# Performance work log

Hardware: AMD Instinct MI355X
Metric: run time of the kernel (lower is better)

## Reference

```python
import jax, jax.numpy as jnp
import numpy as np

DIRECTIONS = [(0, 0), (1, 0), (-1, 0), (0, 1), (0, -1)]  # (dx, dy)
BN_EPS = 1e-5


def shift2d(x, directions=DIRECTIONS):
    # x: (B, C, H, W). Split channels into G groups, roll each spatially,
    # zero out the wrapped-around border (zero_pad mode), then concat.
    C = x.shape[1]
    G = len(directions)
    base = C // G
    sizes = [base] * (G - 1) + [C - base * (G - 1)]
    starts = np.concatenate([[0], np.cumsum(sizes)])
    out = []
    for i, (dx, dy) in enumerate(directions):
        chunk = x[:, starts[i]:starts[i + 1]]
        if dx == 0 and dy == 0:
            out.append(chunk)
            continue
        y = jnp.roll(chunk, shift=(dy, dx), axis=(-2, -1))
        if dy > 0:
            y = y.at[..., :dy, :].set(0.0)
        elif dy < 0:
            y = y.at[..., dy:, :].set(0.0)
        if dx > 0:
            y = y.at[..., :, :dx].set(0.0)
        elif dx < 0:
            y = y.at[..., :, dx:].set(0.0)
        out.append(y)
    return jnp.concatenate(out, axis=1)


def setup_inputs() -> dict:
    key = jax.random.key(0)
    k1, k2, k3, k4 = jax.random.split(key, 4)
    B, Cin, Cout, H, W = 32, 256, 256, 56, 56
    x = jax.random.normal(k1, (B, Cin, H, W), dtype=jnp.float32)
    pw_w = jax.random.normal(k2, (Cout, Cin), dtype=jnp.float32) * (1.0 / np.sqrt(Cin))
    gamma = jnp.ones((Cout,), dtype=jnp.float32)
    beta = jnp.zeros((Cout,), dtype=jnp.float32)
    running_mean = jax.random.normal(k3, (Cout,), dtype=jnp.float32) * 0.1
    running_var = jax.random.uniform(k4, (Cout,), dtype=jnp.float32, minval=0.5, maxval=1.5)
    return {"x": x, "pw_w": pw_w, "gamma": gamma, "beta": beta,
            "running_mean": running_mean, "running_var": running_var}


def reference(x, pw_w, gamma, beta, running_mean, running_var):
    # Shift (parameter-free spatial mixing)
    y = shift2d(x)
    # stride=1 -> down is Identity
    # 1x1 conv (no bias): pointwise channel mixing
    y = jnp.einsum('bchw,oc->bohw', y, pw_w)
    # BatchNorm2d (inference form with running stats) + ReLU
    inv = gamma * jax.lax.rsqrt(running_var + BN_EPS)
    y = y * inv[None, :, None, None] + (beta - running_mean * inv)[None, :, None, None]
    return jax.nn.relu(y)
```

## Files before the change

kernel.cpp:

```cpp
#include <hip/hip_runtime.h>

#define H_ 56
#define W_ 56
#define HW_ 3136
#define CIN_ 256
#define COUT_ 256

typedef __attribute__((ext_vector_type(8))) short short8;
typedef __attribute__((ext_vector_type(4))) float f32x4;

__device__ unsigned short g_wbf[COUT_ * CIN_];

__device__ __forceinline__ int swz32(int n) { return ((n ^ (n >> 3)) & 3) << 3; }

__device__ __forceinline__ unsigned short f2bf(float f) {
  union { float f; unsigned int i; } v; v.f = f;
  unsigned int b = v.i + (0x7fffu + ((v.i >> 16) & 1u));
  return (unsigned short)(b >> 16);
}

__device__ __forceinline__ void gload_lds16(const unsigned short* g, unsigned short* l) {
  __builtin_amdgcn_global_load_lds(
      (const __attribute__((address_space(1))) unsigned int*)g,
      (__attribute__((address_space(3))) unsigned int*)l, 16, 0, 0);
}

__device__ __forceinline__ void shift_decode(int c, int& dx, int& dy) {
  if (c < 102)      { dy = 0; dx = (c < 51) ? 0 : 1; }
  else if (c < 153) { dx = -1; dy = 0; }
  else if (c < 204) { dx = 0;  dy = 1; }
  else              { dx = 0;  dy = -1; }
}

__global__ __launch_bounds__(256)
void prep_weights(const float* __restrict__ wgt) {
  int idx  = blockIdx.x * 256 + threadIdx.x;
  int tile = idx >> 12;
  int bm = tile >> 3, kt = tile & 7;
  int e   = idx & 4095;
  int m   = e >> 5, col = e & 31;
  int o   = bm * 128 + m;
  int k   = kt * 32 + (col ^ swz32(m));
  g_wbf[idx] = f2bf(wgt[o * CIN_ + k]);
}

__device__ __forceinline__ void load_x(const float* __restrict__ x, size_t xb,
                                       int hh, int w0, int c,
                                       float4& p0, float4& p1, float& pe) {
  int dx, dy; shift_decode(c, dx, dy);
  int h2 = hh - dy;
  p0 = make_float4(0.f, 0.f, 0.f, 0.f);
  p1 = make_float4(0.f, 0.f, 0.f, 0.f);
  pe = 0.f;
  if ((unsigned)h2 < (unsigned)H_) {
    const float* row = x + xb + (size_t)c * HW_ + h2 * W_;
    p0 = *(const float4*)(row + w0);
    p1 = *(const float4*)(row + w0 + 4);
    if (dx == 1)       { if (w0 > 0)      pe = row[w0 - 1]; }
    else if (dx == -1) { if (w0 + 8 < W_) pe = row[w0 + 8]; }
  }
}

__device__ __forceinline__ void write_b(unsigned short* __restrict__ B,
                                        int nloc0, int krow, int c,
                                        const float4& p0, const float4& p1, float pe) {
  int dx, dy; shift_decode(c, dx, dy);
  float s[8] = {p0.x, p0.y, p0.z, p0.w, p1.x, p1.y, p1.z, p1.w};
  float vals[8];
  if (dx == 0) {
    #pragma unroll
    for (int i = 0; i < 8; ++i) vals[i] = s[i];
  } else if (dx == 1) {
    #pragma unroll
    for (int i = 7; i >= 1; --i) vals[i] = s[i - 1];
    vals[0] = pe;
  } else {
    #pragma unroll
    for (int i = 0; i < 7; ++i) vals[i] = s[i + 1];
    vals[7] = pe;
  }
  #pragma unroll
  for (int i = 0; i < 8; ++i) {
    int nl = nloc0 + i;
    B[nl * 32 + (krow ^ swz32(nl))] = f2bf(vals[i]);
  }
}

__global__ __launch_bounds__(256, 6)
void shiftconv_gemm(const float* __restrict__ x,
                    const float* __restrict__ gamma,
                    const float* __restrict__ beta,
                    const float* __restrict__ rmean,
                    const float* __restrict__ rvar,
                    float* __restrict__ out)
{
  __shared__ unsigned short Alds[2][128 * 32];
  __shared__ unsigned short Blds[2][64 * 32];
  __shared__ float bnp[256];

  const int t = threadIdx.x;
  const int orig = blockIdx.x;
  const int wgid = (orig & 7) * 392 + (orig >> 3);
  const int bm   = wgid & 1;
  const int bn   = wgid >> 1;

  const int lane = t & 63;
  const int wv   = t >> 6;
  const int wm   = wv >> 1;
  const int wn   = wv & 1;
  const int quad = lane >> 4;
  const int l15  = lane & 15;

  if (t < 128) {
    int o = bm * 128 + t;
    float inv = gamma[o] * rsqrtf(rvar[o] + 1e-5f);
    bnp[2 * t]     = inv;
    bnp[2 * t + 1] = beta[o] - rmean[o] * inv;
  }

  const int chunk  = t & 7;
  const int krow   = t >> 3;
  const int nloc0  = chunk * 8;
  const int nglob0 = bn * 64 + nloc0;
  const int bidx   = nglob0 / HW_;
  const int rem    = nglob0 - bidx * HW_;
  const int hh     = rem / W_;
  const int w0     = rem - hh * W_;
  const size_t xb  = (size_t)bidx * CIN_ * HW_;

  const unsigned short* wsrc = g_wbf + bm * (8 * 4096) + t * 8;

  f32x4 acc[4][2];
  #pragma unroll
  for (int i = 0; i < 4; ++i)
    #pragma unroll
    for (int j = 0; j < 2; ++j)
      acc[i][j] = (f32x4){0.f, 0.f, 0.f, 0.f};

  float4 p0, p1;
  float  pe;

  {
    const unsigned short* g = wsrc;
    gload_lds16(g,        &Alds[0][wv * 512]);
    gload_lds16(g + 2048, &Alds[0][wv * 512 + 2048]);
  }
  load_x(x, xb, hh, w0, krow, p0, p1, pe);
  write_b(&Blds[0][0], nloc0, krow, krow, p0, p1, pe);
  __syncthreads();

  const int kb = quad * 8;
  int buf = 0;

  for (int kt = 0; kt < 8; ++kt) {
    if (kt < 7) {
      const unsigned short* g = wsrc + (kt + 1) * 4096;
      gload_lds16(g,        &Alds[buf ^ 1][wv * 512]);
      gload_lds16(g + 2048, &Alds[buf ^ 1][wv * 512 + 2048]);
      load_x(x, xb, hh, w0, (kt + 1) * 32 + krow, p0, p1, pe);
    }

    short8 af[4], bfr[2];
    #pragma unroll
    for (int f = 0; f < 4; ++f) {
      int ml = wm * 64 + f * 16 + l15;
      af[f] = *(const short8*)(&Alds[buf][ml * 32 + (kb ^ swz32(ml))]);
    }
    #pragma unroll
    for (int g2 = 0; g2 < 2; ++g2) {
      int nl = wn * 32 + g2 * 16 + l15;
      bfr[g2] = *(const short8*)(&Blds[buf][nl * 32 + (kb ^ swz32(nl))]);
    }
    #pragma unroll
    for (int mf = 0; mf < 4; ++mf)
      #pragma unroll
      for (int nf = 0; nf < 2; ++nf)
        acc[mf][nf] = __builtin_amdgcn_mfma_f32_16x16x32_bf16(
            af[mf], bfr[nf], acc[mf][nf], 0, 0, 0);

    if (kt < 7)
      write_b(&Blds[buf ^ 1][0], nloc0, krow, (kt + 1) * 32 + krow, p0, p1, pe);

    __syncthreads();
    buf ^= 1;
  }

  size_t nbase[2];
  #pragma unroll
  for (int nf = 0; nf < 2; ++nf) {
    int ng  = bn * 64 + wn * 32 + nf * 16 + l15;
    int b2  = ng / HW_;
    int hw2 = ng - b2 * HW_;
    nbase[nf] = (size_t)b2 * COUT_ * HW_ + hw2;
  }
  #pragma unroll
  for (int mf = 0; mf < 4; ++mf) {
    int mloc = wm * 64 + mf * 16 + quad * 4;
    float inv[4], add[4];
    #pragma unroll
    for (int r = 0; r < 4; ++r) {
      inv[r] = bnp[2 * (mloc + r)];
      add[r] = bnp[2 * (mloc + r) + 1];
    }
    size_t obase = (size_t)(bm * 128 + mloc) * HW_;
    #pragma unroll
    for (int nf = 0; nf < 2; ++nf) {
      #pragma unroll
      for (int r = 0; r < 4; ++r) {
        float v = fmaf(acc[mf][nf][r], inv[r], add[r]);
        out[nbase[nf] + obase + (size_t)r * HW_] = fmaxf(v, 0.0f);
      }
    }
  }
}

extern "C" void kernel_launch(void* const* d_in, const int* in_sizes, int n_in,
                              void* d_out, int out_size, void* d_ws, size_t ws_size,
                              hipStream_t stream) {
  const float* x     = (const float*)d_in[0];
  const float* wgt   = (const float*)d_in[1];
  const float* gamma = (const float*)d_in[2];
  const float* beta  = (const float*)d_in[3];
  const float* rmean = (const float*)d_in[4];
  const float* rvar  = (const float*)d_in[5];
  float* out = (float*)d_out;

  prep_weights<<<dim3(256), dim3(256), 0, stream>>>(wgt);
  shiftconv_gemm<<<dim3(3136), dim3(256), 0, stream>>>(x, gamma, beta, rmean, rvar, out);
}
```

Measured before the change: 222.4 us.

## Restructure B-tile staging to per-pixel scalar loads with packed LDS stores

Each thread now owns one spatial pixel and eight consecutive input channels instead of eight consecutive pixels and one channel. It loads eight scalar floats, which are coalesced across the wavefront along the pixel dimension, and writes them to LDS as a single 16-byte packed store instead of eight scattered 2-byte stores. This removes the float4 edge-handling logic and the LDS store fan-out. In exchange there are more global load instructions per thread and per-element bounds checks. The occupancy hint in launch bounds is also lowered from 6 to 4 waves.

```diff
diff --git a/kernel.cpp b/kernel.cpp
--- a/kernel.cpp
+++ b/kernel.cpp
@@ -44,49 +44,7 @@
   g_wbf[idx] = f2bf(wgt[o * CIN_ + k]);
 }
 
-__device__ __forceinline__ void load_x(const float* __restrict__ x, size_t xb,
-                                       int hh, int w0, int c,
-                                       float4& p0, float4& p1, float& pe) {
-  int dx, dy; shift_decode(c, dx, dy);
-  int h2 = hh - dy;
-  p0 = make_float4(0.f, 0.f, 0.f, 0.f);
-  p1 = make_float4(0.f, 0.f, 0.f, 0.f);
-  pe = 0.f;
-  if ((unsigned)h2 < (unsigned)H_) {
-    const float* row = x + xb + (size_t)c * HW_ + h2 * W_;
-    p0 = *(const float4*)(row + w0);
-    p1 = *(const float4*)(row + w0 + 4);
-    if (dx == 1)       { if (w0 > 0)      pe = row[w0 - 1]; }
-    else if (dx == -1) { if (w0 + 8 < W_) pe = row[w0 + 8]; }
-  }
-}
-
-__device__ __forceinline__ void write_b(unsigned short* __restrict__ B,
-                                        int nloc0, int krow, int c,
-                                        const float4& p0, const float4& p1, float pe) {
-  int dx, dy; shift_decode(c, dx, dy);
-  float s[8] = {p0.x, p0.y, p0.z, p0.w, p1.x, p1.y, p1.z, p1.w};
-  float vals[8];
-  if (dx == 0) {
-    #pragma unroll
-    for (int i = 0; i < 8; ++i) vals[i] = s[i];
-  } else if (dx == 1) {
-    #pragma unroll
-    for (int i = 7; i >= 1; --i) vals[i] = s[i - 1];
-    vals[0] = pe;
-  } else {
-    #pragma unroll
-    for (int i = 0; i < 7; ++i) vals[i] = s[i + 1];
-    vals[7] = pe;
-  }
-  #pragma unroll
-  for (int i = 0; i < 8; ++i) {
-    int nl = nloc0 + i;
-    B[nl * 32 + (krow ^ swz32(nl))] = f2bf(vals[i]);
-  }
-}
-
-__global__ __launch_bounds__(256, 6)
+__global__ __launch_bounds__(256, 4)
 void shiftconv_gemm(const float* __restrict__ x,
                     const float* __restrict__ gamma,
                     const float* __restrict__ beta,
@@ -118,15 +76,16 @@
     bnp[2 * t + 1] = beta[o] - rmean[o] * inv;
   }
 
-  const int chunk  = t & 7;
-  const int krow   = t >> 3;
-  const int nloc0  = chunk * 8;
-  const int nglob0 = bn * 64 + nloc0;
-  const int bidx   = nglob0 / HW_;
-  const int rem    = nglob0 - bidx * HW_;
-  const int hh     = rem / W_;
-  const int w0     = rem - hh * W_;
-  const size_t xb  = (size_t)bidx * CIN_ * HW_;
+  const int nl    = t & 63;
+  const int kk    = (t >> 6) * 8;
+  const int nglob = bn * 64 + nl;
+  const int bidx  = nglob / HW_;
+  const int rem   = nglob - bidx * HW_;
+  const int hh    = rem / W_;
+  const int ww    = rem - hh * W_;
+  const size_t xb = (size_t)bidx * CIN_ * HW_;
+  unsigned short* bdst0 = &Blds[0][nl * 32 + (kk ^ swz32(nl))];
+  unsigned short* bdst1 = &Blds[1][nl * 32 + (kk ^ swz32(nl))];
 
   const unsigned short* wsrc = g_wbf + bm * (8 * 4096) + t * 8;
 
@@ -137,16 +96,34 @@
     for (int j = 0; j < 2; ++j)
       acc[i][j] = (f32x4){0.f, 0.f, 0.f, 0.f};
 
-  float4 p0, p1;
-  float  pe;
+  float fv[8];
+
+  auto loadB = [&](int ktile) {
+    #pragma unroll
+    for (int j = 0; j < 8; ++j) {
+      int c = ktile * 32 + kk + j;
+      int dx, dy; shift_decode(c, dx, dy);
+      int h2 = hh - dy, w2 = ww - dx;
+      float v = 0.f;
+      if ((unsigned)h2 < (unsigned)H_ && (unsigned)w2 < (unsigned)W_)
+        v = x[xb + (size_t)c * HW_ + h2 * W_ + w2];
+      fv[j] = v;
+    }
+  };
+  auto writeB = [&](unsigned short* dst) {
+    union { short8 v; unsigned short s[8]; } pk;
+    #pragma unroll
+    for (int j = 0; j < 8; ++j) pk.s[j] = f2bf(fv[j]);
+    *(short8*)dst = pk.v;
+  };
 
   {
     const unsigned short* g = wsrc;
     gload_lds16(g,        &Alds[0][wv * 512]);
     gload_lds16(g + 2048, &Alds[0][wv * 512 + 2048]);
   }
-  load_x(x, xb, hh, w0, krow, p0, p1, pe);
-  write_b(&Blds[0][0], nloc0, krow, krow, p0, p1, pe);
+  loadB(0);
+  writeB(bdst0);
   __syncthreads();
 
   const int kb = quad * 8;
@@ -157,7 +134,7 @@
       const unsigned short* g = wsrc + (kt + 1) * 4096;
       gload_lds16(g,        &Alds[buf ^ 1][wv * 512]);
       gload_lds16(g + 2048, &Alds[buf ^ 1][wv * 512 + 2048]);
-      load_x(x, xb, hh, w0, (kt + 1) * 32 + krow, p0, p1, pe);
+      loadB(kt + 1);
     }
 
     short8 af[4], bfr[2];
@@ -168,8 +145,8 @@
     }
     #pragma unroll
     for (int g2 = 0; g2 < 2; ++g2) {
-      int nl = wn * 32 + g2 * 16 + l15;
-      bfr[g2] = *(const short8*)(&Blds[buf][nl * 32 + (kb ^ swz32(nl))]);
+      int nl2 = wn * 32 + g2 * 16 + l15;
+      bfr[g2] = *(const short8*)(&Blds[buf][nl2 * 32 + (kb ^ swz32(nl2))]);
     }
     #pragma unroll
     for (int mf = 0; mf < 4; ++mf)
@@ -179,7 +156,7 @@
             af[mf], bfr[nf], acc[mf][nf], 0, 0, 0);
 
     if (kt < 7)
-      write_b(&Blds[buf ^ 1][0], nloc0, krow, (kt + 1) * 32 + krow, p0, p1, pe);
+      writeB((buf ^ 1) ? bdst1 : bdst0);
 
     __syncthreads();
     buf ^= 1;
```

Result: faster. 210.7 us (-5.3%).
